# Kernel optimization log

Measured on AMD Instinct MI355X. Metric: run time of the kernel, lower is better.

## Reference

```python
import jax, jax.numpy as jnp
import numpy as np
from jax import lax

EGO, MEM, NOBJ = 64, 128, 20
EPS = 1e-5

def gru_cell(x, h, w_ih, w_hh, b_ih, b_hh):
    # x: [..., EGO], h: [..., MEM]; torch GRUCell gate order r,z,n
    gi = jnp.einsum('...c,gc->...g', x, w_ih) + b_ih
    gh = jnp.einsum('...c,gc->...g', h, w_hh) + b_hh
    ir, iz, inn = jnp.split(gi, 3, axis=-1)
    hr, hz, hn = jnp.split(gh, 3, axis=-1)
    r = jax.nn.sigmoid(ir + hr)
    z = jax.nn.sigmoid(iz + hz)
    n = jnp.tanh(inn + r * hn)
    return (1.0 - z) * n + z * h

def conv(x, w, pad):
    return lax.conv_general_dilated(x, w, (1, 1), [(pad, pad), (pad, pad)],
                                    dimension_numbers=('NCHW', 'OIHW', 'NCHW'))

def bn(x, g, b):
    # training-mode BatchNorm2d: batch stats over (N,H,W)
    mu = jnp.mean(x, axis=(0, 2, 3), keepdims=True)
    var = jnp.var(x, axis=(0, 2, 3), keepdims=True)
    return (x - mu) * lax.rsqrt(var + EPS) * g[None, :, None, None] + b[None, :, None, None]

def setup_inputs() -> dict:
    key = jax.random.key(0)
    ks = jax.random.split(key, 16)
    noise = 0.01
    inp = {
        'features': jax.random.normal(ks[0], (2, 4, 256, 256, EGO), jnp.float32),
        'masks_inliers': jax.random.randint(ks[1], (2, 4, 256, 256), 0, 2, jnp.int32),
        'w_ih': jax.random.uniform(ks[2], (3 * MEM, EGO), jnp.float32, -noise, noise),
        'w_hh': jax.random.uniform(ks[3], (3 * MEM, MEM), jnp.float32, -noise, noise),
        'b_ih': jax.random.uniform(ks[4], (3 * MEM,), jnp.float32, -noise, noise),
        'b_hh': jnp.zeros((3 * MEM,), jnp.float32),
        'conv1_w': jax.random.normal(ks[5], (128, MEM, 7, 7), jnp.float32) * 0.02,
        'bn1_g': jnp.ones((128,), jnp.float32), 'bn1_b': jnp.zeros((128,), jnp.float32),
        'conv2_w': jax.random.normal(ks[6], (64, 128, 3, 3), jnp.float32) * 0.02,
        'bn2_g': jnp.ones((64,), jnp.float32), 'bn2_b': jnp.zeros((64,), jnp.float32),
        'conv3_w': jax.random.normal(ks[7], (48, 64, 3, 3), jnp.float32) * 0.02,
        'bn3_g': jnp.ones((48,), jnp.float32), 'bn3_b': jnp.zeros((48,), jnp.float32),
        'obj1_w': jax.random.normal(ks[8], (48, 48, 3, 3), jnp.float32) * 0.02,
        'bn4_g': jnp.ones((48,), jnp.float32), 'bn4_b': jnp.zeros((48,), jnp.float32),
        'obj2_w': jax.random.normal(ks[9], (NOBJ, 48, 1, 1), jnp.float32) * 0.02,
        'obj2_b': jnp.zeros((NOBJ,), jnp.float32),
    }
    return inp

def reference(features, masks_inliers, w_ih, w_hh, b_ih, b_hh,
              conv1_w, bn1_g, bn1_b, conv2_w, bn2_g, bn2_b,
              conv3_w, bn3_g, bn3_b, obj1_w, bn4_g, bn4_b, obj2_w, obj2_b):
    N = features.shape[0]
    state0 = jnp.zeros((N, 256, 256, MEM), jnp.float32)
    obs0 = jnp.zeros((N, 256, 256), jnp.int32)

    feats_t = jnp.moveaxis(features, 1, 0)       # [T,N,256,256,EGO]
    masks_t = jnp.moveaxis(masks_inliers, 1, 0)  # [T,N,256,256]

    def step(carry, xs):
        state, obs = carry
        feat, inl = xs
        m = inl > 0                               # [N,256,256]
        any_n = jnp.any(m, axis=(1, 2))           # [N]
        new_state = gru_cell(feat, state, w_ih, w_hh, b_ih, b_hh)
        state = jnp.where(m[..., None], new_state, state)
        obs = obs + inl * any_n[:, None, None].astype(inl.dtype)
        return (state, obs), None

    (state, observed_masks), _ = lax.scan(step, (state0, obs0), (feats_t, masks_t))

    memory = jnp.transpose(state, (0, 3, 1, 2))   # NCHW
    # decoder
    x = jax.nn.relu(bn(conv(memory, conv1_w, 3), bn1_g, bn1_b))
    x = jax.nn.relu(bn(conv(x, conv2_w, 1), bn2_g, bn2_b))
    x = jax.nn.relu(bn(conv(x, conv3_w, 1), bn3_g, bn3_b))
    x = jax.nn.relu(bn(conv(x, obj1_w, 1), bn4_g, bn4_b))
    semmap = conv(x, obj2_w, 0) + obj2_b[None, :, None, None]
    return semmap, observed_masks
```

## Files before the change

### kernel.cpp

```cpp
#include <hip/hip_runtime.h>
#include <hip/hip_bf16.h>
#include <math.h>

#define HWSZ 65536
#define NPIX 131072
#define LDA 208

typedef __attribute__((ext_vector_type(8))) short short8;
typedef __attribute__((ext_vector_type(4))) float f32x4;
typedef __attribute__((ext_vector_type(16))) float f32x16;

__device__ __forceinline__ float sigmf(float x){ return 1.f/(1.f+__expf(-x)); }
__device__ __forceinline__ float tanhf2(float x){
  x = fminf(fmaxf(x,-15.f),15.f);
  float e = __expf(2.f*x);
  return (e-1.f)/(e+1.f);
}
__device__ __forceinline__ unsigned short f2b(float f){
  __hip_bfloat16 b = __float2bfloat16(f);
  return *(unsigned short*)&b;
}
__device__ __forceinline__ float b2f(unsigned short u){
  unsigned int v = ((unsigned int)u)<<16;
  return __uint_as_float(v);
}

__global__ void prep_gru_wb(const float* __restrict__ wih, const float* __restrict__ whh,
                            unsigned short* __restrict__ WG){
  int idx = blockIdx.x*256+threadIdx.x;
  if(idx >= 6*384*32) return;
  int kq = idx&31; int r = idx>>5;
  int c = r%384; int ch = r/384;
  int k = ch*32+kq;
  float v = (k<64) ? wih[c*64+k] : whh[c*128+(k-64)];
  WG[idx] = f2b(v);
}

__global__ void prep_conv_w(const float* __restrict__ src, unsigned short* __restrict__ dst,
                            int IC, int ICC, int OC, int KS, int total){
  int idx = blockIdx.x*256+threadIdx.x;
  if(idx>=total) return;
  int icq = idx&31; int r = idx>>5;
  int oc = r%OC; r/=OC;
  int ch = r%ICC; int tap = r/ICC;
  int ky = tap/KS, kx = tap%KS;
  int ic = ch*32+icq;
  float v = (ic<IC)? src[((oc*IC+ic)*KS+ky)*KS+kx] : 0.f;
  dst[idx] = f2b(v);
}

__global__ void prep_conv_w32(const float* __restrict__ src, unsigned short* __restrict__ dst,
                              int IC, int OC, int KS, int total){
  int idx = blockIdx.x*256+threadIdx.x;
  if(idx>=total) return;
  int q = idx&15; int r = idx>>4;
  int oc = r%OC; r/=OC;
  int ICC = IC/16;
  int ch = r%ICC; int tap = r/ICC;
  int ky = tap/KS, kx = tap%KS;
  int ic = ch*16+q;
  dst[idx] = f2b(src[((oc*IC+ic)*KS+ky)*KS+kx]);
}

__global__ void flags_kernel(const int* __restrict__ masks, int* __restrict__ flags){
  __shared__ int red[256];
  int b = blockIdx.x; int acc=0;
  const int* m = masks + b*HWSZ;
  for(int i=threadIdx.x;i<HWSZ;i+=256) acc |= (m[i]>0)?1:0;
  red[threadIdx.x]=acc; __syncthreads();
  for(int s=128;s>0;s>>=1){ if(threadIdx.x<s) red[threadIdx.x]|=red[threadIdx.x+s]; __syncthreads(); }
  if(threadIdx.x==0) flags[b]=red[0];
}

__global__ void obs_kernel(const int* __restrict__ masks, const int* __restrict__ flags,
                           float* __restrict__ out){
  int p = blockIdx.x*256+threadIdx.x;
  if(p>=NPIX) return;
  int n = p>>16, hw = p&65535;
  int s=0;
  #pragma unroll
  for(int t=0;t<4;t++) s += masks[((n*4+t)<<16)+hw]*flags[n*4+t];
  out[p]=(float)s;
}

__launch_bounds__(512,4)
__global__ void gru_mfma(const float* __restrict__ feat, const int* __restrict__ masks,
                         const unsigned short* __restrict__ WG,
                         const float* __restrict__ bih, const float* __restrict__ bhh,
                         unsigned short* __restrict__ S){
  __shared__ __align__(16) unsigned short ax[32*LDA];
  __shared__ int msk[32];
  const int tid=threadIdx.x, wv=tid>>6, lane=tid&63, l15=lane&15, quad=lane>>4;
  const int p0=blockIdx.x*32;
  const int n=p0>>16, hw0=p0&65535;
  const int j16=wv*16;

  const int j=j16+l15;
  const float brv = bih[j]     + bhh[j];
  const float bzv = bih[128+j] + bhh[128+j];
  const float binv= bih[256+j];
  const float bhnv= bhh[256+j];

  float4 z4={0.f,0.f,0.f,0.f};
  { int px=tid>>4, c8=tid&15; *(float4*)&ax[px*LDA+64+c8*8]=z4; }

  for(int t=0;t<4;t++){
    __syncthreads();
    { int px=tid>>4, c4=tid&15;
      float4 v=*(const float4*)&feat[(size_t)(((n*4+t)<<16)|(hw0+px))*64 + c4*4];
      ushort4 u; u.x=f2b(v.x);u.y=f2b(v.y);u.z=f2b(v.z);u.w=f2b(v.w);
      *(ushort4*)&ax[px*LDA+c4*4]=u;
    }
    if(tid<32) msk[tid]=masks[((n*4+t)<<16)+hw0+tid];
    __syncthreads();

    f32x4 aR[2],aZ[2],aNX[2],aNH[2];
    #pragma unroll
    for(int mt=0;mt<2;mt++){
      f32x4 zz={0.f,0.f,0.f,0.f};
      aR[mt]=zz; aZ[mt]=zz; aNX[mt]=zz; aNH[mt]=zz;
    }

    #pragma unroll
    for(int ch=0;ch<6;ch++){
      short8 a[2];
      #pragma unroll
      for(int mt=0;mt<2;mt++)
        a[mt]=*(const short8*)&ax[(mt*16+l15)*LDA + ch*32 + quad*8];
      const unsigned short* bb = WG + (((size_t)(ch*384 + l15))<<5) + quad*8;
      short8 bR=*(const short8*)(bb + (((size_t)(     j16))<<5));
      short8 bZ=*(const short8*)(bb + (((size_t)(128+j16))<<5));
      short8 bN=*(const short8*)(bb + (((size_t)(256+j16))<<5));
      #pragma unroll
      for(int mt=0;mt<2;mt++){
        aR[mt]=__builtin_amdgcn_mfma_f32_16x16x32_bf16(a[mt],bR,aR[mt],0,0,0);
        aZ[mt]=__builtin_amdgcn_mfma_f32_16x16x32_bf16(a[mt],bZ,aZ[mt],0,0,0);
        if(ch<2)
          aNX[mt]=__builtin_amdgcn_mfma_f32_16x16x32_bf16(a[mt],bN,aNX[mt],0,0,0);
        else
          aNH[mt]=__builtin_amdgcn_mfma_f32_16x16x32_bf16(a[mt],bN,aNH[mt],0,0,0);
      }
    }
    __syncthreads();

    #pragma unroll
    for(int mt=0;mt<2;mt++){
      #pragma unroll
      for(int r=0;r<4;r++){
        int px=mt*16+quad*4+r;
        float rg=sigmf(aR[mt][r]+brv);
        float zg=sigmf(aZ[mt][r]+bzv);
        float nn=tanhf2(aNX[mt][r]+binv+rg*(aNH[mt][r]+bhnv));
        unsigned short hu=ax[px*LDA+64+j];
        float hold=b2f(hu);
        float h2=(1.f-zg)*nn+zg*hold;
        ax[px*LDA+64+j] = (msk[px]>0)? f2b(h2) : hu;
      }
    }
  }
  __syncthreads();
  { int px=tid>>4, c8=tid&15;
    *(float4*)&S[(size_t)(p0+px)*128 + c8*8] = *(float4*)&ax[px*LDA+64+c8*8];
  }
}

template<int IC,int OC,int KS>
__launch_bounds__(256,3)
__global__ void m32conv(const unsigned short* __restrict__ in, const unsigned short* __restrict__ Wb,
                        unsigned short* __restrict__ out, float* __restrict__ partials){
  constexpr int P=KS/2, ROWS=128+KS-1, LDR=IC+8, ICC=IC/16, C8=IC/8;
  constexpr int NTW=OC/32, NS=KS*ICC;
  __shared__ __align__(16) unsigned short lds[ROWS*LDR];
  const int tid=threadIdx.x;
  const int wv=tid>>6, lane=tid&63, l31=lane&31, hf=lane>>5;
  const int p0=blockIdx.x*128;
  const int n=p0>>16; const int hw0=p0&65535; const int y0=hw0>>8, x0=hw0&255;
  const int m0=wv*32;

  f32x16 acc[NTW];
  #pragma unroll
  for(int nn=0;nn<NTW;nn++){
    #pragma unroll
    for(int r=0;r<16;r++) acc[nn][r]=0.f;
  }

  for(int ky=0;ky<KS;ky++){
    int ys=y0+ky-P;
    if(ys<0||ys>255) continue;
    __syncthreads();
    for(int i=tid;i<ROWS*C8;i+=256){
      int c8=i%C8, px=i/C8;
      int xg=x0-P+px;
      float4 v={0.f,0.f,0.f,0.f};
      if(xg>=0 && xg<256)
        v = *(const float4*)(in + (size_t)(((n<<16)|(ys<<8))+xg)*IC + c8*8);
      *(float4*)&lds[px*LDR + c8*8] = v;
    }
    __syncthreads();

    short8 Bn[NTW];
    {
      const unsigned short* bp = Wb + (((size_t)((ky*KS+0)*ICC+0)*OC + l31)<<4) + hf*8;
      #pragma unroll
      for(int nn=0;nn<NTW;nn++) Bn[nn]=*(const short8*)(bp + (nn<<9));
    }
    #pragma unroll
    for(int s=0;s<NS;s++){
      const int kx=s/ICC, ch=s%ICC;
      short8 Bc[NTW];
      #pragma unroll
      for(int nn=0;nn<NTW;nn++) Bc[nn]=Bn[nn];
      if(s+1<NS){
        const int kx2=(s+1)/ICC, ch2=(s+1)%ICC;
        const unsigned short* bp = Wb + (((size_t)((ky*KS+kx2)*ICC+ch2)*OC + l31)<<4) + hf*8;
        #pragma unroll
        for(int nn=0;nn<NTW;nn++) Bn[nn]=*(const short8*)(bp + (nn<<9));
      }
      short8 a = *(const short8*)&lds[(m0 + l31 + kx)*LDR + ch*16 + hf*8];
      #pragma unroll
      for(int nn=0;nn<NTW;nn++)
        acc[nn]=__builtin_amdgcn_mfma_f32_32x32x16_bf16(a,Bc[nn],acc[nn],0,0,0);
    }
  }
  __syncthreads();

  #pragma unroll
  for(int nn=0;nn<NTW;nn++){
    int oc = nn*32 + l31;
    #pragma unroll
    for(int r=0;r<16;r++){
      int m = (r&3) + 8*(r>>2) + 4*hf;
      out[(size_t)(p0+m0+m)*OC + oc] = f2b(acc[nn][r]);
    }
  }

  float* ps=(float*)lds;
  int rps = wv*2+hf;
  #pragma unroll
  for(int nn=0;nn<NTW;nn++){
    float s1=0.f,s2=0.f;
    #pragma unroll
    for(int r=0;r<16;r++){ float v=acc[nn][r]; s1+=v; s2+=v*v; }
    ps[rps*OC + nn*32+l31]=s1;
    ps[(8+rps)*OC + nn*32+l31]=s2;
  }
  __syncthreads();
  if(tid<OC){
    float t1=0.f,t2=0.f;
    #pragma unroll
    for(int g=0;g<8;g++){ t1+=ps[g*OC+tid]; t2+=ps[(8+g)*OC+tid]; }
    partials[(size_t)blockIdx.x*2*OC+tid]=t1;
    partials[(size_t)blockIdx.x*2*OC+OC+tid]=t2;
  }
}

template<int IC,int ICP,int OC,int KS,int TPB,int WM,int WN>
__launch_bounds__(TPB, (TPB==512)?4:3)
__global__ void mconv(const unsigned short* __restrict__ in, const unsigned short* __restrict__ Wb,
                      unsigned short* __restrict__ out, float* __restrict__ partials){
  constexpr int P=KS/2, ROWS=128+KS-1, LDR=ICP+8, ICC=ICP/32, C8=ICP/8;
  constexpr int MT = 128/(WM*16);
  constexpr int OCW = OC/WN;
  constexpr int NTW = OCW/16;
  constexpr int NS = KS*ICC;
  constexpr int RPS = WM*4;
  __shared__ __align__(16) unsigned short lds[ROWS*LDR];
  const int tid=threadIdx.x;
  const int wv=tid>>6, lane=tid&63, l15=lane&15, quad=lane>>4;
  const int wm=wv/WN, wn=wv%WN;
  const int p0=blockIdx.x*128;
  const int n=p0>>16; const int hw0=p0&65535; const int y0=hw0>>8, x0=hw0&255;

  f32x4 acc[MT][NTW];
  #pragma unroll
  for(int mt=0;mt<MT;mt++)
    #pragma unroll
    for(int nn=0;nn<NTW;nn++){ f32x4 z={0.f,0.f,0.f,0.f}; acc[mt][nn]=z; }

  for(int ky=0;ky<KS;ky++){
    int ys=y0+ky-P;
    if(ys<0||ys>255) continue;
    __syncthreads();
    for(int i=tid;i<ROWS*C8;i+=TPB){
      int c8=i%C8, px=i/C8;
      int xg=x0-P+px;
      float4 v={0.f,0.f,0.f,0.f};
      if(xg>=0 && xg<256 && c8*8<IC)
        v = *(const float4*)(in + (size_t)(((n<<16)|(ys<<8))+xg)*IC + c8*8);
      *(float4*)&lds[px*LDR + c8*8] = v;
    }
    __syncthreads();

    short8 Bn[NTW];
    {
      const unsigned short* bp = Wb + ((size_t)(((ky*KS+0)*ICC+0)*OC + wn*OCW + l15)<<5) + quad*8;
      #pragma unroll
      for(int nn=0;nn<NTW;nn++) Bn[nn]=*(const short8*)(bp + (nn<<9));
    }
    #pragma unroll
    for(int s=0;s<NS;s++){
      const int kx=s/ICC, ch=s%ICC;
      short8 Bc[NTW];
      #pragma unroll
      for(int nn=0;nn<NTW;nn++) Bc[nn]=Bn[nn];
      if(s+1<NS){
        const int kx2=(s+1)/ICC, ch2=(s+1)%ICC;
        const unsigned short* bp = Wb + ((size_t)(((ky*KS+kx2)*ICC+ch2)*OC + wn*OCW + l15)<<5) + quad*8;
        #pragma unroll
        for(int nn=0;nn<NTW;nn++) Bn[nn]=*(const short8*)(bp + (nn<<9));
      }
      short8 a[MT];
      #pragma unroll
      for(int mt=0;mt<MT;mt++)
        a[mt]=*(const short8*)&lds[(wm*(MT*16) + mt*16 + l15 + kx)*LDR + ch*32 + quad*8];
      #pragma unroll
      for(int mt=0;mt<MT;mt++)
        #pragma unroll
        for(int nn=0;nn<NTW;nn++)
          acc[mt][nn]=__builtin_amdgcn_mfma_f32_16x16x32_bf16(a[mt],Bc[nn],acc[mt][nn],0,0,0);
    }
  }
  __syncthreads();

  #pragma unroll
  for(int mt=0;mt<MT;mt++){
    int pxb = p0 + wm*(MT*16) + mt*16 + quad*4;
    #pragma unroll
    for(int nn=0;nn<NTW;nn++){
      int oc = wn*OCW + nn*16 + l15;
      #pragma unroll
      for(int r=0;r<4;r++)
        out[(size_t)(pxb+r)*OC + oc] = f2b(acc[mt][nn][r]);
    }
  }

  float* ps=(float*)lds;
  int rps = wm*4+quad;
  #pragma unroll
  for(int nn=0;nn<NTW;nn++){
    float s1=0.f,s2=0.f;
    #pragma unroll
    for(int mt=0;mt<MT;mt++)
      #pragma unroll
      for(int r=0;r<4;r++){ float v=acc[mt][nn][r]; s1+=v; s2+=v*v; }
    ps[rps*OC + wn*OCW + nn*16+l15]=s1;
    ps[(RPS+rps)*OC + wn*OCW + nn*16+l15]=s2;
  }
  __syncthreads();
  if(tid<OC){
    float t1=0.f,t2=0.f;
    #pragma unroll
    for(int g=0;g<RPS;g++){ t1+=ps[g*OC+tid]; t2+=ps[(RPS+g)*OC+tid]; }
    partials[(size_t)blockIdx.x*2*OC+tid]=t1;
    partials[(size_t)blockIdx.x*2*OC+OC+tid]=t2;
  }
}

__global__ void stats_kernel(const float* __restrict__ partials, const float* __restrict__ g,
                             const float* __restrict__ b, float2* __restrict__ stats, int OC, int NB){
  __shared__ float r1[256], r2[256];
  int oc=blockIdx.x; int tid=threadIdx.x;
  float s1=0.f,s2=0.f;
  for(int bl=tid;bl<NB;bl+=256){ s1+=partials[(size_t)bl*2*OC+oc]; s2+=partials[(size_t)bl*2*OC+OC+oc]; }
  r1[tid]=s1;r2[tid]=s2; __syncthreads();
  for(int s=128;s>0;s>>=1){ if(tid<s){r1[tid]+=r1[tid+s]; r2[tid]+=r2[tid+s];} __syncthreads(); }
  if(tid==0){
    float mean=r1[0]*(1.f/131072.f);
    float var =r2[0]*(1.f/131072.f)-mean*mean;
    float sc=g[oc]*rsqrtf(var+1e-5f);
    float2 st; st.x=sc; st.y=b[oc]-mean*sc;
    stats[oc]=st;
  }
}

__global__ void bnrelu_b2b(const unsigned short* __restrict__ src, unsigned short* __restrict__ dst,
                           const float2* __restrict__ stats, int OC8, int total8){
  for(int i=blockIdx.x*256+threadIdx.x;i<total8;i+=gridDim.x*256){
    int c8=i%OC8;
    float4 v=((const float4*)src)[i];
    const unsigned short* us=(const unsigned short*)&v;
    float4 o;
    unsigned short* od=(unsigned short*)&o;
    #pragma unroll
    for(int j=0;j<8;j++){
      float2 s=stats[c8*8+j];
      od[j]=f2b(fmaxf(0.f, b2f(us[j])*s.x+s.y));
    }
    ((float4*)dst)[i]=o;
  }
}

__global__ void obj2_kernel(const unsigned short* __restrict__ in, const float* __restrict__ w,
                            const float* __restrict__ bias, float* __restrict__ out){
  __shared__ float wsm[20*48];
  __shared__ float bs[20];
  int tid=threadIdx.x;
  for(int i=tid;i<20*48;i+=256) wsm[i]=w[i];
  if(tid<20) bs[tid]=bias[tid];
  __syncthreads();
  int p=blockIdx.x*256+tid;
  int n=p>>16, hw=p&65535;
  float x[48];
  #pragma unroll
  for(int i=0;i<6;i++){
    float4 v=*(const float4*)&in[(size_t)p*48+i*8];
    const unsigned short* us=(const unsigned short*)&v;
    #pragma unroll
    for(int j=0;j<8;j++) x[i*8+j]=b2f(us[j]);
  }
  #pragma unroll
  for(int o=0;o<20;o++){
    float s=bs[o];
    #pragma unroll
    for(int c=0;c<48;c++) s+=x[c]*wsm[o*48+c];
    out[(size_t)((n*20+o)<<16)+hw]=s;
  }
}

extern "C" void kernel_launch(void* const* d_in, const int* in_sizes, int n_in,
                              void* d_out, int out_size, void* d_ws, size_t ws_size,
                              hipStream_t stream) {
  const float* feat = (const float*)d_in[0];
  const int*   masks= (const int*)  d_in[1];
  const float* w_ih = (const float*)d_in[2];
  const float* w_hh = (const float*)d_in[3];
  const float* b_ih = (const float*)d_in[4];
  const float* b_hh = (const float*)d_in[5];
  const float* c1w  = (const float*)d_in[6];
  const float* bn1g = (const float*)d_in[7];  const float* bn1b=(const float*)d_in[8];
  const float* c2w  = (const float*)d_in[9];
  const float* bn2g = (const float*)d_in[10]; const float* bn2b=(const float*)d_in[11];
  const float* c3w  = (const float*)d_in[12];
  const float* bn3g = (const float*)d_in[13]; const float* bn3b=(const float*)d_in[14];
  const float* o1w  = (const float*)d_in[15];
  const float* bn4g = (const float*)d_in[16]; const float* bn4b=(const float*)d_in[17];
  const float* o2w  = (const float*)d_in[18]; const float* o2b =(const float*)d_in[19];

  char* ws = (char*)d_ws;
  unsigned short* Rb  = (unsigned short*)(ws + 0);
  unsigned short* A1b = (unsigned short*)(ws + 33554432);
  unsigned short* A3b = A1b;
  unsigned short* Sb  = (unsigned short*)(ws + 67108864);
  unsigned short* A2b = Sb;
  unsigned short* A4b = Sb;
  unsigned short* W1b = (unsigned short*)(ws + 100663296);
  unsigned short* W2b = (unsigned short*)(ws + 102268928);
  unsigned short* W3b = (unsigned short*)(ws + 102416384);
  unsigned short* W4b = (unsigned short*)(ws + 102471680);
  unsigned short* WGb = (unsigned short*)(ws + 102526976);
  float* partials = (float*)(ws + 102674432);
  float2* stats   = (float2*)(ws + 103723008);
  int*   flags    = (int*)  (ws + 103724032);

  float* semmap = (float*)d_out;
  float* obsout = (float*)d_out + 2621440;

  prep_gru_wb<<<288,256,0,stream>>>(w_ih,w_hh,WGb);
  prep_conv_w32<<<(49*8*128*16+255)/256,256,0,stream>>>(c1w,W1b,128,128,7,49*8*128*16);
  prep_conv_w32<<<(9*8*64*16 +255)/256,256,0,stream>>>(c2w,W2b,128,64,3,9*8*64*16);
  prep_conv_w<<<(9*2*48*32 +255)/256,256,0,stream>>>(c3w,W3b,64,2,48,3,9*2*48*32);
  prep_conv_w<<<(9*2*48*32 +255)/256,256,0,stream>>>(o1w,W4b,48,2,48,3,9*2*48*32);

  flags_kernel<<<8,256,0,stream>>>(masks,flags);
  obs_kernel<<<512,256,0,stream>>>(masks,flags,obsout);

  gru_mfma<<<4096,512,0,stream>>>(feat,masks,WGb,b_ih,b_hh,Sb);

  m32conv<128,128,7><<<1024,256,0,stream>>>(Sb,W1b,Rb,partials);
  stats_kernel<<<128,256,0,stream>>>(partials,bn1g,bn1b,stats,128,1024);
  bnrelu_b2b<<<4096,256,0,stream>>>(Rb,A1b,stats,16,NPIX*128/8);

  m32conv<128,64,3><<<1024,256,0,stream>>>(A1b,W2b,Rb,partials);
  stats_kernel<<<64,256,0,stream>>>(partials,bn2g,bn2b,stats,64,1024);
  bnrelu_b2b<<<4096,256,0,stream>>>(Rb,A2b,stats,8,NPIX*64/8);

  mconv<64,64,48,3,256,4,1><<<1024,256,0,stream>>>(A2b,W3b,Rb,partials);
  stats_kernel<<<48,256,0,stream>>>(partials,bn3g,bn3b,stats,48,1024);
  bnrelu_b2b<<<4096,256,0,stream>>>(Rb,A3b,stats,6,NPIX*48/8);

  mconv<48,64,48,3,256,4,1><<<1024,256,0,stream>>>(A3b,W4b,Rb,partials);
  stats_kernel<<<48,256,0,stream>>>(partials,bn4g,bn4b,stats,48,1024);
  bnrelu_b2b<<<4096,256,0,stream>>>(Rb,A4b,stats,6,NPIX*48/8);

  obj2_kernel<<<512,256,0,stream>>>(A4b,o2w,o2b,semmap);
}
```

Before: 810.9 us.

## Retile m32conv warps into a 2x2 grid over pixels and output channels

Each of the four waves in the m32conv kernel used to own 32 pixel rows and all output channels. Now the waves form a 2x2 grid: each owns 64 pixel rows (two 32-row MFMA tiles) and half of the output channels. Each wave loads half as many weight fragments per step from global memory and reuses each fragment across two A tiles, which cuts global weight traffic per MFMA. The cost is extra LDS A loads per wave and a rework of the partial-stats reduction from 8 to 4 row groups per channel.

```diff
diff --git a/kernel.cpp b/kernel.cpp
--- a/kernel.cpp
+++ b/kernel.cpp
@@ -169,20 +169,23 @@
 __global__ void m32conv(const unsigned short* __restrict__ in, const unsigned short* __restrict__ Wb,
                         unsigned short* __restrict__ out, float* __restrict__ partials){
   constexpr int P=KS/2, ROWS=128+KS-1, LDR=IC+8, ICC=IC/16, C8=IC/8;
-  constexpr int NTW=OC/32, NS=KS*ICC;
+  constexpr int OCW=OC/2, NTW=OCW/32, NS=KS*ICC;
   __shared__ __align__(16) unsigned short lds[ROWS*LDR];
   const int tid=threadIdx.x;
   const int wv=tid>>6, lane=tid&63, l31=lane&31, hf=lane>>5;
+  const int wm=wv>>1, wn=wv&1;
   const int p0=blockIdx.x*128;
   const int n=p0>>16; const int hw0=p0&65535; const int y0=hw0>>8, x0=hw0&255;
-  const int m0=wv*32;
-
-  f32x16 acc[NTW];
-  #pragma unroll
-  for(int nn=0;nn<NTW;nn++){
-    #pragma unroll
-    for(int r=0;r<16;r++) acc[nn][r]=0.f;
-  }
+  const int m0=wm*64;
+
+  f32x16 acc[2][NTW];
+  #pragma unroll
+  for(int mt=0;mt<2;mt++)
+    #pragma unroll
+    for(int nn=0;nn<NTW;nn++){
+      #pragma unroll
+      for(int r=0;r<16;r++) acc[mt][nn][r]=0.f;
+    }
 
   for(int ky=0;ky<KS;ky++){
     int ys=y0+ky-P;
@@ -200,7 +203,7 @@
 
     short8 Bn[NTW];
     {
-      const unsigned short* bp = Wb + (((size_t)((ky*KS+0)*ICC+0)*OC + l31)<<4) + hf*8;
+      const unsigned short* bp = Wb + (((size_t)((ky*KS+0)*ICC+0)*OC + wn*OCW + l31)<<4) + hf*8;
       #pragma unroll
       for(int nn=0;nn<NTW;nn++) Bn[nn]=*(const short8*)(bp + (nn<<9));
     }
@@ -212,43 +215,53 @@
       for(int nn=0;nn<NTW;nn++) Bc[nn]=Bn[nn];
       if(s+1<NS){
         const int kx2=(s+1)/ICC, ch2=(s+1)%ICC;
-        const unsigned short* bp = Wb + (((size_t)((ky*KS+kx2)*ICC+ch2)*OC + l31)<<4) + hf*8;
+        const unsigned short* bp = Wb + (((size_t)((ky*KS+kx2)*ICC+ch2)*OC + wn*OCW + l31)<<4) + hf*8;
         #pragma unroll
         for(int nn=0;nn<NTW;nn++) Bn[nn]=*(const short8*)(bp + (nn<<9));
       }
-      short8 a = *(const short8*)&lds[(m0 + l31 + kx)*LDR + ch*16 + hf*8];
-      #pragma unroll
-      for(int nn=0;nn<NTW;nn++)
-        acc[nn]=__builtin_amdgcn_mfma_f32_32x32x16_bf16(a,Bc[nn],acc[nn],0,0,0);
-    }
-  }
-  __syncthreads();
-
-  #pragma unroll
-  for(int nn=0;nn<NTW;nn++){
-    int oc = nn*32 + l31;
-    #pragma unroll
-    for(int r=0;r<16;r++){
-      int m = (r&3) + 8*(r>>2) + 4*hf;
-      out[(size_t)(p0+m0+m)*OC + oc] = f2b(acc[nn][r]);
+      short8 a[2];
+      #pragma unroll
+      for(int mt=0;mt<2;mt++)
+        a[mt] = *(const short8*)&lds[(m0 + mt*32 + l31 + kx)*LDR + ch*16 + hf*8];
+      #pragma unroll
+      for(int mt=0;mt<2;mt++)
+        #pragma unroll
+        for(int nn=0;nn<NTW;nn++)
+          acc[mt][nn]=__builtin_amdgcn_mfma_f32_32x32x16_bf16(a[mt],Bc[nn],acc[mt][nn],0,0,0);
+    }
+  }
+  __syncthreads();
+
+  #pragma unroll
+  for(int mt=0;mt<2;mt++){
+    #pragma unroll
+    for(int nn=0;nn<NTW;nn++){
+      int oc = wn*OCW + nn*32 + l31;
+      #pragma unroll
+      for(int r=0;r<16;r++){
+        int m = (r&3) + 8*(r>>2) + 4*hf;
+        out[(size_t)(p0+m0+mt*32+m)*OC + oc] = f2b(acc[mt][nn][r]);
+      }
     }
   }
 
   float* ps=(float*)lds;
-  int rps = wv*2+hf;
+  int rps = wm*2+hf;
   #pragma unroll
   for(int nn=0;nn<NTW;nn++){
     float s1=0.f,s2=0.f;
     #pragma unroll
-    for(int r=0;r<16;r++){ float v=acc[nn][r]; s1+=v; s2+=v*v; }
-    ps[rps*OC + nn*32+l31]=s1;
-    ps[(8+rps)*OC + nn*32+l31]=s2;
+    for(int mt=0;mt<2;mt++)
+      #pragma unroll
+      for(int r=0;r<16;r++){ float v=acc[mt][nn][r]; s1+=v; s2+=v*v; }
+    ps[rps*OC + wn*OCW + nn*32+l31]=s1;
+    ps[(4+rps)*OC + wn*OCW + nn*32+l31]=s2;
   }
   __syncthreads();
   if(tid<OC){
     float t1=0.f,t2=0.f;
     #pragma unroll
-    for(int g=0;g<8;g++){ t1+=ps[g*OC+tid]; t2+=ps[(8+g)*OC+tid]; }
+    for(int g=0;g<4;g++){ t1+=ps[g*OC+tid]; t2+=ps[(4+g)*OC+tid]; }
     partials[(size_t)blockIdx.x*2*OC+tid]=t1;
     partials[(size_t)blockIdx.x*2*OC+OC+tid]=t2;
   }
```

New measurement: 773.9 us. -4.6%, faster.
